# Kernel tuning notes

Measured on AMD Instinct MI355X. Metric: run time of the kernel, lower is better.

The kernel has to match this reference:

```python
import jax, jax.numpy as jnp
import numpy as np

B, T, U, V = 4, 300, 80, 1024
DE, DD, INNER = 320, 320, 512


def setup_inputs() -> dict:
    key = jax.random.key(0)
    ks = jax.random.split(key, 6)
    enc_state = jax.random.normal(ks[0], (B, T, DE), jnp.float32)
    dec_state = jax.random.normal(ks[1], (B, U + 1, DD), jnp.float32)
    Wf = jax.random.normal(ks[2], (INNER, DE + DD), jnp.float32) / np.float32(np.sqrt(DE + DD))
    bf = jnp.zeros((INNER,), jnp.float32)
    Wp = jax.random.normal(ks[3], (V, INNER), jnp.float32) / np.float32(np.sqrt(INNER))
    bp = jnp.zeros((V,), jnp.float32)
    targets = jax.random.randint(ks[4], (B, U), 1, V).astype(jnp.int32)  # labels avoid blank=0
    inputs_length = jnp.full((B,), T, jnp.int32)
    targets_length = jnp.full((B,), U, jnp.int32)
    return {"enc_state": enc_state, "dec_state": dec_state, "Wf": Wf, "bf": bf,
            "Wp": Wp, "bp": bp, "targets": targets,
            "inputs_length": inputs_length, "targets_length": targets_length}


def joint_logits(enc, dec, Wf, bf, Wp, bp):
    # Linear over concat([enc, dec]) == Linear(enc) + Linear(dec): avoids materializing the concat.
    de = enc.shape[-1]
    Wf_e, Wf_d = Wf[:, :de], Wf[:, de:]
    enc_p = jnp.einsum('btd,id->bti', enc, Wf_e)   # [B,T,inner]
    dec_p = jnp.einsum('bud,id->bui', dec, Wf_d)   # [B,U1,inner]
    h = jnp.tanh(enc_p[:, :, None, :] + dec_p[:, None, :, :] + bf)  # [B,T,U1,inner]
    return jnp.einsum('btui,vi->btuv', h, Wp) + bp  # [B,T,U1,V]


def rnnt_loss(log_probs, targets, t_len, u_len):
    # log_probs: [B,T,U1,V], blank index 0.
    lp_blank = log_probs[..., 0]  # [B,T,U1]
    lp_emit = jnp.take_along_axis(log_probs[:, :, :-1, :], targets[:, None, :, None], axis=3)[..., 0]  # [B,T,U]
    # row0: alpha[0,u] = sum_{k<u} emit[0,k]
    row0 = jnp.pad(jnp.cumsum(lp_emit[:, 0, :], axis=-1), ((0, 0), (1, 0)))  # [B,U1]

    def outer(alpha_prev, xs):
        blank_prev, emit_cur = xs  # [B,U1], [B,U]
        first = alpha_prev[:, 0] + blank_prev[:, 0]  # [B]

        def inner(c, x):
            a_plus_b, e = x  # [B],[B]
            c2 = jnp.logaddexp(a_plus_b, c + e)
            return c2, c2
        xs_in = ((alpha_prev[:, 1:] + blank_prev[:, 1:]).T, emit_cur.T)  # [U,B]
        _, rest = jax.lax.scan(inner, first, xs_in)  # [U,B]
        row = jnp.concatenate([first[None, :], rest], axis=0).T  # [B,U1]
        return row, row

    xs = (jnp.swapaxes(lp_blank[:, :-1, :], 0, 1), jnp.swapaxes(lp_emit[:, 1:, :], 0, 1))
    _, rows = jax.lax.scan(outer, row0, xs)  # [T-1,B,U1]
    alpha = jnp.concatenate([row0[None], rows], axis=0)  # [T,B,U1]
    bidx = jnp.arange(alpha.shape[1])
    ll = alpha[t_len - 1, bidx, u_len] + lp_blank[bidx, t_len - 1, u_len]
    return -jnp.mean(ll)


def reference(enc_state, dec_state, Wf, bf, Wp, bp, targets, inputs_length, targets_length):
    logits = joint_logits(enc_state, dec_state, Wf, bf, Wp, bp).astype(jnp.float32)
    log_probs = jax.nn.log_softmax(logits, axis=-1)
    return rnnt_loss(log_probs, targets, inputs_length, targets_length)
```

## Files before the change

kernel.cpp:

```cpp
#include <hip/hip_runtime.h>

#define B_DIM 4
#define T_DIM 300
#define U_DIM 80
#define UP1   81
#define V_DIM 1024
#define NINNER 512
#define NROWS (B_DIM * T_DIM * UP1)
#define EP_ROWS (B_DIM * T_DIM)
#define DP_ROWS (B_DIM * UP1)
#define NDIAG_B 380
#define NDIAG_E 379
#define WF_PART 163840
#define LOG2E 1.44269504088896341f
#define LN2   0.69314718055994531f

typedef float f32x4 __attribute__((ext_vector_type(4)));
typedef short short8 __attribute__((ext_vector_type(8)));
typedef short short4v __attribute__((ext_vector_type(4)));
typedef __bf16 bf16x8 __attribute__((ext_vector_type(8)));

static __device__ __forceinline__ short f2bf(float f) {
  return (short)__builtin_bit_cast(unsigned short, (__bf16)f);
}
static __device__ __forceinline__ float bf2f(short s) {
  unsigned int u = ((unsigned int)(unsigned short)s) << 16;
  return __builtin_bit_cast(float, u);
}
static __device__ __forceinline__ float tanh_fast(float x) {
  float e = __builtin_amdgcn_exp2f(x * 2.88539008177792681f);
  return 1.0f - 2.0f * __builtin_amdgcn_rcpf(e + 1.0f);
}
static __device__ __forceinline__ float lse2_2(float a, float b) {
  float mx = fmaxf(a, b), mn = fminf(a, b);
  return mx + __builtin_amdgcn_logf(1.0f + __builtin_amdgcn_exp2f(mn - mx));
}

__global__ __launch_bounds__(256) void cvt_kernel(
    const float* __restrict__ Wf, const float* __restrict__ Wp,
    short* __restrict__ WfB, short* __restrict__ WpB) {
  int idx = blockIdx.x * 256 + threadIdx.x;
  const int nf = (512 * 640) / 4;
  const int np = (V_DIM * NINNER) / 4;
  if (idx < nf) {
    float4 v = ((const float4*)Wf)[idx];
    int flat = idx * 4;
    int c = flat / 640;
    int kc = flat - c * 640;
    int part = (kc >= 320);
    int k0 = kc - (part ? 320 : 0);
    int dest = (part ? WF_PART : 0)
             + ((c >> 4) * 10 + (k0 >> 5)) * 512
             + (((k0 >> 3) & 3) * 16 + (c & 15)) * 8 + (k0 & 7);
    short4v o;
    o[0] = f2bf(v.x); o[1] = f2bf(v.y); o[2] = f2bf(v.z); o[3] = f2bf(v.w);
    *(short4v*)(WfB + dest) = o;
  } else if (idx < nf + np) {
    int j = idx - nf;
    float4 v = ((const float4*)Wp)[j];
    int flat = j * 4;
    int c = flat >> 9;
    int k0 = flat & 511;
    int dest = ((c >> 4) * 16 + (k0 >> 5)) * 512
             + (((k0 >> 3) & 3) * 16 + (c & 15)) * 8 + (k0 & 7);
    short4v o;
    o[0] = f2bf(v.x); o[1] = f2bf(v.y); o[2] = f2bf(v.z); o[3] = f2bf(v.w);
    *(short4v*)(WpB + dest) = o;
  }
}

#define EP_BLOCKS 19
__global__ __launch_bounds__(256) void proj_kernel(
    const float* __restrict__ enc, const float* __restrict__ dec,
    const short* __restrict__ WfB, const float* __restrict__ bfv,
    short* __restrict__ epB, short* __restrict__ dpB) {
  const int half = blockIdx.x & 1;
  const int ob = blockIdx.x >> 1;
  const bool is_dp = (ob >= EP_BLOCKS);
  const int row0 = (is_dp ? ob - EP_BLOCKS : ob) * 64;
  const int nrows = is_dp ? DP_ROWS : EP_ROWS;
  const float* __restrict__ src = is_dp ? dec : enc;
  const short* __restrict__ bb = WfB + (is_dp ? WF_PART : 0);
  short* __restrict__ out = is_dp ? dpB : epB;

  __shared__ short As[64 * 320];
  const int tid = threadIdx.x;

  #pragma unroll
  for (int it = 0; it < 10; ++it) {
    int chunk = it * 256 + tid;
    int m = chunk / 40;
    int c = chunk - m * 40;
    int r = row0 + m;
    short8 hv;
    #pragma unroll
    for (int j = 0; j < 8; ++j) hv[j] = 0;
    if (r < nrows) {
      const float* p = src + (size_t)r * 320 + c * 8;
      float4 a0 = *(const float4*)p;
      float4 a1 = *(const float4*)(p + 4);
      hv[0] = f2bf(a0.x); hv[1] = f2bf(a0.y); hv[2] = f2bf(a0.z); hv[3] = f2bf(a0.w);
      hv[4] = f2bf(a1.x); hv[5] = f2bf(a1.y); hv[6] = f2bf(a1.z); hv[7] = f2bf(a1.w);
    }
    int off = (m * 640 + c * 16) ^ ((m & 7) << 4);
    *(short8*)((char*)As + off) = hv;
  }
  __syncthreads();

  const int lane = tid & 63, wid = tid >> 6;
  const int lr = lane & 15, g = lane >> 4;

  int lin[4], xm[4];
  #pragma unroll
  for (int mf = 0; mf < 4; ++mf) {
    int row = mf * 16 + lr;
    lin[mf] = row * 640 + g * 16;
    xm[mf] = (row & 7) << 4;
  }

  const int n0 = half * 256 + wid * 64;
  const short* bptr[4];
  float bfc[4];
  #pragma unroll
  for (int nf2 = 0; nf2 < 4; ++nf2) {
    bptr[nf2] = bb + (n0 / 16 + nf2) * 5120 + lane * 8;
    bfc[nf2] = is_dp ? bfv[n0 + nf2 * 16 + lr] : 0.f;
  }
  f32x4 acc[4][4];
  #pragma unroll
  for (int mf = 0; mf < 4; ++mf)
    #pragma unroll
    for (int nf2 = 0; nf2 < 4; ++nf2)
      acc[mf][nf2] = (f32x4){0.f, 0.f, 0.f, 0.f};

  #pragma unroll 2
  for (int kk = 0; kk < 10; ++kk) {
    bf16x8 av[4], bv[4];
    #pragma unroll
    for (int mf = 0; mf < 4; ++mf) {
      int off = (lin[mf] + (kk << 6)) ^ xm[mf];
      av[mf] = __builtin_bit_cast(bf16x8, *(const short8*)((const char*)As + off));
    }
    #pragma unroll
    for (int nf2 = 0; nf2 < 4; ++nf2)
      bv[nf2] = __builtin_bit_cast(bf16x8, *(const short8*)(bptr[nf2] + kk * 512));
    #pragma unroll
    for (int mf = 0; mf < 4; ++mf)
      #pragma unroll
      for (int nf2 = 0; nf2 < 4; ++nf2)
        acc[mf][nf2] = __builtin_amdgcn_mfma_f32_16x16x32_bf16(av[mf], bv[nf2], acc[mf][nf2], 0, 0, 0);
  }
  #pragma unroll
  for (int mf = 0; mf < 4; ++mf)
    #pragma unroll
    for (int nf2 = 0; nf2 < 4; ++nf2)
      #pragma unroll
      for (int rr = 0; rr < 4; ++rr) {
        int rowl = mf * 16 + g * 4 + rr;
        int grow = row0 + rowl;
        if (grow < nrows) {
          int col = n0 + nf2 * 16 + lr;
          out[(size_t)grow * NINNER + col] = f2bf(acc[mf][nf2][rr] + bfc[nf2]);
        }
      }
}

#define JROWS 64
__global__ __launch_bounds__(512) void joint_kernel(
    const short* __restrict__ epB, const short* __restrict__ dpB,
    const short* __restrict__ WpB, const float* __restrict__ bp,
    const int* __restrict__ tgt,
    float* __restrict__ lpb_d, float* __restrict__ lpe_d) {
  extern __shared__ char hbuf[];
  __shared__ int ep_off[JROWS], dp_off[JROWS], bld_off[JROWS], eld_off[JROWS], tgt_s[JROWS];
  __shared__ float l0_s[JROWS], lt_s[JROWS];
  __shared__ float ws_s[8][JROWS];

  const int tid = threadIdx.x;
  const int row0 = blockIdx.x * JROWS;

  if (tid < JROWS) {
    int gr = row0 + tid;
    if (gr < NROWS) {
      int b = gr / (T_DIM * UP1);
      int rem = gr - b * (T_DIM * UP1);
      int t = rem / UP1;
      int u = rem - t * UP1;
      ep_off[tid] = (b * T_DIM + t) * NINNER;
      dp_off[tid] = (b * UP1 + u) * NINNER;
      bld_off[tid] = (b * NDIAG_B + (t + u)) * UP1 + u;
      eld_off[tid] = (u < U_DIM) ? ((b * NDIAG_E + (t + u)) * U_DIM + u) : -1;
      tgt_s[tid] = (u < U_DIM) ? tgt[b * U_DIM + u] : 0;
    } else {
      ep_off[tid] = 0; dp_off[tid] = 0; bld_off[tid] = -1; eld_off[tid] = -1; tgt_s[tid] = 0;
    }
    l0_s[tid] = 0.f; lt_s[tid] = 0.f;
  }
  __syncthreads();

  #pragma unroll 2
  for (int it = 0; it < 8; ++it) {
    int chunk = it * 512 + tid;
    int m = chunk >> 6, c = chunk & 63;
    short8 hv;
    #pragma unroll
    for (int j = 0; j < 8; ++j) hv[j] = 0;
    if (bld_off[m] >= 0) {
      short8 ev = *(const short8*)(epB + ep_off[m] + c * 8);
      short8 dv = *(const short8*)(dpB + dp_off[m] + c * 8);
      #pragma unroll
      for (int j = 0; j < 8; ++j)
        hv[j] = f2bf(tanh_fast(bf2f(ev[j]) + bf2f(dv[j])));
    }
    int off = ((m << 10) + (c << 4)) ^ ((m & 7) << 4);
    *(short8*)(hbuf + off) = hv;
  }
  __syncthreads();

  const int lane = tid & 63, wid = tid >> 6;
  const int lr = lane & 15, g = lane >> 4;

  int lin[4], xm[4];
  #pragma unroll
  for (int mf = 0; mf < 4; ++mf) {
    int row = mf * 16 + lr;
    lin[mf] = (row << 10) + (g << 4);
    xm[mf] = (row & 7) << 4;
  }
  int tv[4][4];
  #pragma unroll
  for (int mf = 0; mf < 4; ++mf)
    #pragma unroll
    for (int rr = 0; rr < 4; ++rr)
      tv[mf][rr] = tgt_s[mf * 16 + g * 4 + rr];

  float rsum[4][4];
  #pragma unroll
  for (int mf = 0; mf < 4; ++mf)
    #pragma unroll
    for (int rr = 0; rr < 4; ++rr) rsum[mf][rr] = 0.f;

  #pragma unroll
  for (int sc = 0; sc < 2; ++sc) {
    const int n0 = wid * 128 + sc * 64;
    const short* bptr[4];
    float bpv[4];
    #pragma unroll
    for (int nf = 0; nf < 4; ++nf) {
      bptr[nf] = WpB + (n0 / 16 + nf) * 8192 + lane * 8;
      bpv[nf] = bp[n0 + nf * 16 + lr] * LOG2E;
    }
    f32x4 acc[4][4];
    #pragma unroll
    for (int mf = 0; mf < 4; ++mf)
      #pragma unroll
      for (int nf = 0; nf < 4; ++nf)
        acc[mf][nf] = (f32x4){0.f, 0.f, 0.f, 0.f};

    #pragma unroll 2
    for (int kk = 0; kk < 16; ++kk) {
      bf16x8 av[4], bv[4];
      #pragma unroll
      for (int mf = 0; mf < 4; ++mf) {
        int off = (lin[mf] + (kk << 6)) ^ xm[mf];
        av[mf] = __builtin_bit_cast(bf16x8, *(const short8*)(hbuf + off));
      }
      #pragma unroll
      for (int nf = 0; nf < 4; ++nf)
        bv[nf] = __builtin_bit_cast(bf16x8, *(const short8*)(bptr[nf] + kk * 512));
      __builtin_amdgcn_s_setprio(1);
      #pragma unroll
      for (int mf = 0; mf < 4; ++mf)
        #pragma unroll
        for (int nf = 0; nf < 4; ++nf)
          acc[mf][nf] = __builtin_amdgcn_mfma_f32_16x16x32_bf16(av[mf], bv[nf], acc[mf][nf], 0, 0, 0);
      __builtin_amdgcn_s_setprio(0);
    }
    #pragma unroll
    for (int mf = 0; mf < 4; ++mf)
      #pragma unroll
      for (int rr = 0; rr < 4; ++rr) {
        float x0 = __builtin_fmaf(acc[mf][0][rr], LOG2E, bpv[0]);
        float x1 = __builtin_fmaf(acc[mf][1][rr], LOG2E, bpv[1]);
        float x2 = __builtin_fmaf(acc[mf][2][rr], LOG2E, bpv[2]);
        float x3 = __builtin_fmaf(acc[mf][3][rr], LOG2E, bpv[3]);
        int rowl = mf * 16 + g * 4 + rr;
        if (wid == 0 && sc == 0 && lr == 0) l0_s[rowl] = x0;
        int dtv = tv[mf][rr] - n0;
        if (dtv >= 0 && dtv < 64 && (dtv & 15) == lr) {
          int nfi = dtv >> 4;
          lt_s[rowl] = (nfi == 0) ? x0 : (nfi == 1) ? x1 : (nfi == 2) ? x2 : x3;
        }
        rsum[mf][rr] += __builtin_amdgcn_exp2f(x0) + __builtin_amdgcn_exp2f(x1)
                      + __builtin_amdgcn_exp2f(x2) + __builtin_amdgcn_exp2f(x3);
      }
  }
  #pragma unroll
  for (int mf = 0; mf < 4; ++mf)
    #pragma unroll
    for (int rr = 0; rr < 4; ++rr) {
      float s_ = rsum[mf][rr];
      #pragma unroll
      for (int o = 1; o < 16; o <<= 1) s_ += __shfl_xor(s_, o);
      if (lr == 0) ws_s[wid][mf * 16 + g * 4 + rr] = s_;
    }
  __syncthreads();
  if (tid < JROWS) {
    int bo = bld_off[tid];
    if (bo >= 0) {
      float S = 0.f;
      #pragma unroll
      for (int w = 0; w < 8; ++w) S += ws_s[w][tid];
      float lse2v = __builtin_amdgcn_logf(S);
      lpb_d[bo] = l0_s[tid] - lse2v;
      int eo = eld_off[tid];
      if (eo >= 0) lpe_d[eo] = lt_s[tid] - lse2v;
    }
  }
}

#define ACH 8
#define NCH 48
__global__ __launch_bounds__(256) void alpha_kernel(
    const float* __restrict__ lpb_d, const float* __restrict__ lpe_d,
    const int* __restrict__ ilen, const int* __restrict__ ulen_,
    float* __restrict__ out) {
  __shared__ float lls[B_DIM];
  const int tid = threadIdx.x;
  const int b = tid >> 6;
  const int lane = tid & 63;
  const float NEG = -1e30f;
  const int tl = ilen[b], ul = ulen_[b];
  const int dstar = tl - 1 + ul;

  const int u0 = lane;
  const int u1 = 64 + lane;
  const bool act1 = (u1 <= 80);
  const int uc1 = act1 ? u1 : 80;

  const float* pb = lpb_d + (size_t)b * (NDIAG_B * UP1);
  const float* pe = lpe_d + (size_t)b * (NDIAG_E * U_DIM);

  float Ab0r[ACH], Ab0m[ACH], Ae0r[ACH], Ae0m[ACH];
  float Ab1r[ACH], Ab1m[ACH], Ae1r[ACH], Ae1m[ACH];
  float Bb0r[ACH], Bb0m[ACH], Be0r[ACH], Be0m[ACH];
  float Bb1r[ACH], Bb1m[ACH], Be1r[ACH], Be1m[ACH];

  #define ALOAD(P, c)                                                        \
    {                                                                        \
      _Pragma("unroll")                                                      \
      for (int j = 0; j < ACH; ++j) {                                        \
        int dd = (c) * ACH + j;                                              \
        int ddb = dd < NDIAG_B ? dd : NDIAG_B - 1;                           \
        int dde = dd < NDIAG_E ? dd : NDIAG_E - 1;                           \
        const float* rb_ = pb + ddb * UP1;                                   \
        const float* re_ = pe + dde * U_DIM;                                 \
        P##b0r[j] = rb_[u0];                                                 \
        P##b0m[j] = rb_[u0 - 1];                                             \
        P##e0r[j] = re_[u0 - 1];                                             \
        P##e0m[j] = re_[u0 - 2];                                             \
        P##b1r[j] = rb_[uc1];                                                \
        P##b1m[j] = rb_[uc1 - 1];                                            \
        P##e1r[j] = re_[uc1 - 1];                                            \
        P##e1m[j] = re_[uc1 - 2];                                            \
      }                                                                      \
    }

  #define ACOMP(P, c)                                                        \
    {                                                                        \
      _Pragma("unroll")                                                      \
      for (int q = 0; q < ACH / 2; ++q) {                                    \
        const int j = 2 * q;                                                 \
        const int s1 = (c) * ACH + j + 1;                                    \
        float s0m1 = __shfl(pa0, (lane + 63) & 63);                          \
        float s0m2 = __shfl(pa0, (lane + 62) & 63);                          \
        float s1m1 = __shfl(pa1, (lane + 63) & 63);                          \
        float s1m2 = __shfl(pa1, (lane + 62) & 63);                          \
        float na0, na1;                                                      \
        float b1_0, e1_0, b1_1, e1_1;                                        \
        {                                                        \
          const int u = u0;                                                  \
          const int t1 = s1 - u;                                             \
          float b1 = (t1 >= 1 && t1 <= T_DIM - 1) ? P##b0r[j] : NEG;         \
          float b2 = (t1 >= 0 && t1 <= T_DIM - 2) ? P##b0r[j + 1] : NEG;     \
          float e1 = (t1 >= 0 && t1 <= T_DIM - 1 && u >= 1) ? P##e0r[j] : NEG; \
          float e2 = (t1 >= -1 && t1 <= T_DIM - 2 && u >= 1) ? P##e0r[j + 1] : NEG; \
          float b1m = (t1 >= 0 && t1 <= T_DIM - 2 && u >= 1) ? P##b0m[j] : NEG; \
          float e1m = (t1 >= -1 && t1 <= T_DIM - 2 && u >= 2) ? P##e0m[j] : NEG; \
          b1_0 = b1; e1_0 = e1;                                              \
          float T1 = b1 + b2;                                                \
          float T2 = lse2_2(e1 + b2, b1m + e2);                              \
          float T3 = e1m + e2;                                               \
          float p0 = pa0 + T1;                                               \
          float p1 = (u >= 1) ? s0m1 + T2 : NEG;                             \
          float p2 = (u >= 2) ? s0m2 + T3 : NEG;                             \
          float mx = fmaxf(fmaxf(p0, p1), p2);                               \
          float ss = __builtin_amdgcn_exp2f(p0 - mx)                         \
                   + __builtin_amdgcn_exp2f(p1 - mx)                         \
                   + __builtin_amdgcn_exp2f(p2 - mx);                        \
          na0 = mx + __builtin_amdgcn_logf(ss);                              \
        }                                                                    \
        {                                                        \
          const int t1 = s1 - u1;                                            \
          float b1 = (act1 && t1 >= 1 && t1 <= T_DIM - 1) ? P##b1r[j] : NEG; \
          float b2 = (act1 && t1 >= 0 && t1 <= T_DIM - 2) ? P##b1r[j + 1] : NEG; \
          float e1 = (act1 && t1 >= 0 && t1 <= T_DIM - 1) ? P##e1r[j] : NEG; \
          float e2 = (act1 && t1 >= -1 && t1 <= T_DIM - 2) ? P##e1r[j + 1] : NEG; \
          float b1m = (act1 && t1 >= 0 && t1 <= T_DIM - 2) ? P##b1m[j] : NEG; \
          float e1m = (act1 && t1 >= -1 && t1 <= T_DIM - 2) ? P##e1m[j] : NEG; \
          b1_1 = b1; e1_1 = e1;                                              \
          float pm1 = (lane == 0) ? s0m1 : s1m1;                             \
          float pm2 = (lane <= 1) ? s0m2 : s1m2;                             \
          float T1 = b1 + b2;                                                \
          float T2 = lse2_2(e1 + b2, b1m + e2);                              \
          float T3 = e1m + e2;                                               \
          float p0 = pa1 + T1;                                               \
          float p1 = pm1 + T2;                                               \
          float p2 = pm2 + T3;                                               \
          float mx = fmaxf(fmaxf(p0, p1), p2);                               \
          float ss = __builtin_amdgcn_exp2f(p0 - mx)                         \
                   + __builtin_amdgcn_exp2f(p1 - mx)                         \
                   + __builtin_amdgcn_exp2f(p2 - mx);                        \
          na1 = act1 ? (mx + __builtin_amdgcn_logf(ss)) : NEG;               \
        }                                                                    \
        if (s1 == dstar) {                   \
          float pm1_0 = (u0 >= 1) ? s0m1 : NEG;                              \
          float vo0 = lse2_2(pa0 + b1_0, pm1_0 + e1_0);                      \
          if (u0 == ul) fin = vo0;                                           \
          float pm1_1 = (lane == 0) ? s0m1 : s1m1;                           \
          float vo1 = lse2_2(pa1 + b1_1, pm1_1 + e1_1);                      \
          if (act1 && u1 == ul) fin = vo1;                                   \
        }                                                                    \
        pa0 = na0; pa1 = na1;                                                \
        if (s1 + 1 == dstar) {              \
          if (u0 == ul) fin = pa0;                                           \
          if (act1 && u1 == ul) fin = pa1;                                   \
        }                                                                    \
      }                                                                      \
    }

  float pa0 = (u0 == 0) ? 0.f : NEG;
  float pa1 = NEG;
  float fin = NEG;
  if (dstar == 0 && u0 == ul) fin = pa0;

  ALOAD(A, 0);
  for (int p = 0; p < NCH / 2; ++p) {
    const int cA = 2 * p, cB = 2 * p + 1;
    ALOAD(B, cB);
    ACOMP(A, cA);
    ALOAD(A, cA + 2);
    ACOMP(B, cB);
  }

  #pragma unroll
  for (int o = 32; o; o >>= 1) fin = fmaxf(fin, __shfl_xor(fin, o));
  if (lane == 0) {
    float last = pb[(size_t)dstar * UP1 + ul];
    lls[b] = fin + last;
  }
  __syncthreads();
  if (tid == 0)
    out[0] = -(lls[0] + lls[1] + lls[2] + lls[3]) * (LN2 * 0.25f);
}

extern "C" void kernel_launch(void* const* d_in, const int* in_sizes, int n_in,
                              void* d_out, int out_size, void* d_ws, size_t ws_size,
                              hipStream_t stream) {
  const float* enc = (const float*)d_in[0];
  const float* dec = (const float*)d_in[1];
  const float* Wf  = (const float*)d_in[2];
  const float* bfv = (const float*)d_in[3];
  const float* Wp  = (const float*)d_in[4];
  const float* bp  = (const float*)d_in[5];
  const int* targets = (const int*)d_in[6];
  const int* ilen    = (const int*)d_in[7];
  const int* ulen    = (const int*)d_in[8];
  float* out = (float*)d_out;
  char* ws = (char*)d_ws;

  short* WfB   = (short*)(ws + 0);
  short* WpB   = (short*)(ws + 655360);
  short* epB   = (short*)(ws + 1703936);
  short* dpB   = (short*)(ws + 2932736);
  float* lpb_d = (float*)(ws + 3264512);
  float* lpe_d = (float*)(ws + 3756992);

  cvt_kernel<<<832, 256, 0, stream>>>(Wf, Wp, WfB, WpB);
  proj_kernel<<<50, 256, 0, stream>>>(enc, dec, WfB, bfv, epB, dpB);
  joint_kernel<<<(NROWS + JROWS - 1) / JROWS, 512, 65536, stream>>>(epB, dpB, WpB, bp, targets, lpb_d, lpe_d);
  alpha_kernel<<<1, 256, 0, stream>>>(lpb_d, lpe_d, ilen, ulen, out);
}
```

Measured before the change: 225.4 us.

## Pad diagonal log-prob buffers with NEG sentinels and shrink joint tile to 48 rows

```diff
diff --git a/kernel.cpp b/kernel.cpp
--- a/kernel.cpp
+++ b/kernel.cpp
@@ -11,9 +11,11 @@
 #define DP_ROWS (B_DIM * UP1)
 #define NDIAG_B 380
 #define NDIAG_E 379
+#define DSTRIDE 82
 #define WF_PART 163840
 #define LOG2E 1.44269504088896341f
 #define LN2   0.69314718055994531f
+#define NEGF  -1e30f
 
 typedef float f32x4 __attribute__((ext_vector_type(4)));
 typedef short short8 __attribute__((ext_vector_type(8)));
@@ -34,6 +36,11 @@
 static __device__ __forceinline__ float lse2_2(float a, float b) {
   float mx = fmaxf(a, b), mn = fminf(a, b);
   return mx + __builtin_amdgcn_logf(1.0f + __builtin_amdgcn_exp2f(mn - mx));
+}
+
+__global__ __launch_bounds__(256) void fill_kernel(float* __restrict__ dst, int n4) {
+  int i = blockIdx.x * 256 + threadIdx.x;
+  if (i < n4) ((f32x4*)dst)[i] = (f32x4){NEGF, NEGF, NEGF, NEGF};
 }
 
 __global__ __launch_bounds__(256) void cvt_kernel(
@@ -165,12 +172,12 @@
       }
 }
 
-#define JROWS 64
+#define JROWS 48
 __global__ __launch_bounds__(512) void joint_kernel(
     const short* __restrict__ epB, const short* __restrict__ dpB,
     const short* __restrict__ WpB, const float* __restrict__ bp,
     const int* __restrict__ tgt,
-    float* __restrict__ lpb_d, float* __restrict__ lpe_d) {
+    float* __restrict__ lpb_p, float* __restrict__ lpe_p) {
   extern __shared__ char hbuf[];
   __shared__ int ep_off[JROWS], dp_off[JROWS], bld_off[JROWS], eld_off[JROWS], tgt_s[JROWS];
   __shared__ float l0_s[JROWS], lt_s[JROWS];
@@ -188,8 +195,8 @@
       int u = rem - t * UP1;
       ep_off[tid] = (b * T_DIM + t) * NINNER;
       dp_off[tid] = (b * UP1 + u) * NINNER;
-      bld_off[tid] = (b * NDIAG_B + (t + u)) * UP1 + u;
-      eld_off[tid] = (u < U_DIM) ? ((b * NDIAG_E + (t + u)) * U_DIM + u) : -1;
+      bld_off[tid] = (b * NDIAG_B + (t + u)) * DSTRIDE + 1 + u;
+      eld_off[tid] = (u < U_DIM) ? ((b * NDIAG_E + (t + u)) * DSTRIDE + 2 + u) : -1;
       tgt_s[tid] = (u < U_DIM) ? tgt[b * U_DIM + u] : 0;
     } else {
       ep_off[tid] = 0; dp_off[tid] = 0; bld_off[tid] = -1; eld_off[tid] = -1; tgt_s[tid] = 0;
@@ -199,7 +206,7 @@
   __syncthreads();
 
   #pragma unroll 2
-  for (int it = 0; it < 8; ++it) {
+  for (int it = 0; it < 6; ++it) {
     int chunk = it * 512 + tid;
     int m = chunk >> 6, c = chunk & 63;
     short8 hv;
@@ -220,23 +227,23 @@
   const int lane = tid & 63, wid = tid >> 6;
   const int lr = lane & 15, g = lane >> 4;
 
-  int lin[4], xm[4];
-  #pragma unroll
-  for (int mf = 0; mf < 4; ++mf) {
+  int lin[3], xm[3];
+  #pragma unroll
+  for (int mf = 0; mf < 3; ++mf) {
     int row = mf * 16 + lr;
     lin[mf] = (row << 10) + (g << 4);
     xm[mf] = (row & 7) << 4;
   }
-  int tv[4][4];
-  #pragma unroll
-  for (int mf = 0; mf < 4; ++mf)
+  int tv[3][4];
+  #pragma unroll
+  for (int mf = 0; mf < 3; ++mf)
     #pragma unroll
     for (int rr = 0; rr < 4; ++rr)
       tv[mf][rr] = tgt_s[mf * 16 + g * 4 + rr];
 
-  float rsum[4][4];
-  #pragma unroll
-  for (int mf = 0; mf < 4; ++mf)
+  float rsum[3][4];
+  #pragma unroll
+  for (int mf = 0; mf < 3; ++mf)
     #pragma unroll
     for (int rr = 0; rr < 4; ++rr) rsum[mf][rr] = 0.f;
 
@@ -250,18 +257,18 @@
       bptr[nf] = WpB + (n0 / 16 + nf) * 8192 + lane * 8;
       bpv[nf] = bp[n0 + nf * 16 + lr] * LOG2E;
     }
-    f32x4 acc[4][4];
-    #pragma unroll
-    for (int mf = 0; mf < 4; ++mf)
+    f32x4 acc[3][4];
+    #pragma unroll
+    for (int mf = 0; mf < 3; ++mf)
       #pragma unroll
       for (int nf = 0; nf < 4; ++nf)
         acc[mf][nf] = (f32x4){0.f, 0.f, 0.f, 0.f};
 
     #pragma unroll 2
     for (int kk = 0; kk < 16; ++kk) {
-      bf16x8 av[4], bv[4];
-      #pragma unroll
-      for (int mf = 0; mf < 4; ++mf) {
+      bf16x8 av[3], bv[4];
+      #pragma unroll
+      for (int mf = 0; mf < 3; ++mf) {
         int off = (lin[mf] + (kk << 6)) ^ xm[mf];
         av[mf] = __builtin_bit_cast(bf16x8, *(const short8*)(hbuf + off));
       }
@@ -270,14 +277,14 @@
         bv[nf] = __builtin_bit_cast(bf16x8, *(const short8*)(bptr[nf] + kk * 512));
       __builtin_amdgcn_s_setprio(1);
       #pragma unroll
-      for (int mf = 0; mf < 4; ++mf)
+      for (int mf = 0; mf < 3; ++mf)
         #pragma unroll
         for (int nf = 0; nf < 4; ++nf)
           acc[mf][nf] = __builtin_amdgcn_mfma_f32_16x16x32_bf16(av[mf], bv[nf], acc[mf][nf], 0, 0, 0);
       __builtin_amdgcn_s_setprio(0);
     }
     #pragma unroll
-    for (int mf = 0; mf < 4; ++mf)
+    for (int mf = 0; mf < 3; ++mf)
       #pragma unroll
       for (int rr = 0; rr < 4; ++rr) {
         float x0 = __builtin_fmaf(acc[mf][0][rr], LOG2E, bpv[0]);
@@ -296,7 +303,7 @@
       }
   }
   #pragma unroll
-  for (int mf = 0; mf < 4; ++mf)
+  for (int mf = 0; mf < 3; ++mf)
     #pragma unroll
     for (int rr = 0; rr < 4; ++rr) {
       float s_ = rsum[mf][rr];
@@ -312,9 +319,9 @@
       #pragma unroll
       for (int w = 0; w < 8; ++w) S += ws_s[w][tid];
       float lse2v = __builtin_amdgcn_logf(S);
-      lpb_d[bo] = l0_s[tid] - lse2v;
+      lpb_p[bo] = l0_s[tid] - lse2v;
       int eo = eld_off[tid];
-      if (eo >= 0) lpe_d[eo] = lt_s[tid] - lse2v;
+      if (eo >= 0) lpe_p[eo] = lt_s[tid] - lse2v;
     }
   }
 }
@@ -322,14 +329,14 @@
 #define ACH 8
 #define NCH 48
 __global__ __launch_bounds__(256) void alpha_kernel(
-    const float* __restrict__ lpb_d, const float* __restrict__ lpe_d,
+    const float* __restrict__ lpb_p, const float* __restrict__ lpe_p,
     const int* __restrict__ ilen, const int* __restrict__ ulen_,
     float* __restrict__ out) {
   __shared__ float lls[B_DIM];
   const int tid = threadIdx.x;
   const int b = tid >> 6;
   const int lane = tid & 63;
-  const float NEG = -1e30f;
+  const float NEG = NEGF;
   const int tl = ilen[b], ul = ulen_[b];
   const int dstar = tl - 1 + ul;
 
@@ -338,8 +345,8 @@
   const bool act1 = (u1 <= 80);
   const int uc1 = act1 ? u1 : 80;
 
-  const float* pb = lpb_d + (size_t)b * (NDIAG_B * UP1);
-  const float* pe = lpe_d + (size_t)b * (NDIAG_E * U_DIM);
+  const float* pbb = lpb_p + (size_t)b * (NDIAG_B * DSTRIDE);
+  const float* peb = lpe_p + (size_t)b * (NDIAG_E * DSTRIDE);
 
   float Ab0r[ACH], Ab0m[ACH], Ae0r[ACH], Ae0m[ACH];
   float Ab1r[ACH], Ab1m[ACH], Ae1r[ACH], Ae1m[ACH];
@@ -353,8 +360,8 @@
         int dd = (c) * ACH + j;                                              \
         int ddb = dd < NDIAG_B ? dd : NDIAG_B - 1;                           \
         int dde = dd < NDIAG_E ? dd : NDIAG_E - 1;                           \
-        const float* rb_ = pb + ddb * UP1;                                   \
-        const float* re_ = pe + dde * U_DIM;                                 \
+        const float* rb_ = pbb + ddb * DSTRIDE + 1;                          \
+        const float* re_ = peb + dde * DSTRIDE + 2;                          \
         P##b0r[j] = rb_[u0];                                                 \
         P##b0m[j] = rb_[u0 - 1];                                             \
         P##e0r[j] = re_[u0 - 1];                                             \
@@ -377,38 +384,26 @@
         float s1m1 = __shfl(pa1, (lane + 63) & 63);                          \
         float s1m2 = __shfl(pa1, (lane + 62) & 63);                          \
         float na0, na1;                                                      \
-        float b1_0, e1_0, b1_1, e1_1;                                        \
-        {                                                        \
-          const int u = u0;                                                  \
-          const int t1 = s1 - u;                                             \
-          float b1 = (t1 >= 1 && t1 <= T_DIM - 1) ? P##b0r[j] : NEG;         \
-          float b2 = (t1 >= 0 && t1 <= T_DIM - 2) ? P##b0r[j + 1] : NEG;     \
-          float e1 = (t1 >= 0 && t1 <= T_DIM - 1 && u >= 1) ? P##e0r[j] : NEG; \
-          float e2 = (t1 >= -1 && t1 <= T_DIM - 2 && u >= 1) ? P##e0r[j + 1] : NEG; \
-          float b1m = (t1 >= 0 && t1 <= T_DIM - 2 && u >= 1) ? P##b0m[j] : NEG; \
-          float e1m = (t1 >= -1 && t1 <= T_DIM - 2 && u >= 2) ? P##e0m[j] : NEG; \
-          b1_0 = b1; e1_0 = e1;                                              \
+        {               \
+          float b1 = P##b0r[j], b2 = P##b0r[j + 1];                          \
+          float e1 = P##e0r[j], e2 = P##e0r[j + 1];                          \
+          float b1m = P##b0m[j], e1m = P##e0m[j];                            \
           float T1 = b1 + b2;                                                \
           float T2 = lse2_2(e1 + b2, b1m + e2);                              \
           float T3 = e1m + e2;                                               \
           float p0 = pa0 + T1;                                               \
-          float p1 = (u >= 1) ? s0m1 + T2 : NEG;                             \
-          float p2 = (u >= 2) ? s0m2 + T3 : NEG;                             \
+          float p1 = s0m1 + T2;                                              \
+          float p2 = s0m2 + T3;                                              \
           float mx = fmaxf(fmaxf(p0, p1), p2);                               \
           float ss = __builtin_amdgcn_exp2f(p0 - mx)                         \
                    + __builtin_amdgcn_exp2f(p1 - mx)                         \
                    + __builtin_amdgcn_exp2f(p2 - mx);                        \
-          na0 = mx + __builtin_amdgcn_logf(ss);                              \
+          na0 = fmaxf(mx + __builtin_amdgcn_logf(ss), NEG);                  \
         }                                                                    \
         {                                                        \
-          const int t1 = s1 - u1;                                            \
-          float b1 = (act1 && t1 >= 1 && t1 <= T_DIM - 1) ? P##b1r[j] : NEG; \
-          float b2 = (act1 && t1 >= 0 && t1 <= T_DIM - 2) ? P##b1r[j + 1] : NEG; \
-          float e1 = (act1 && t1 >= 0 && t1 <= T_DIM - 1) ? P##e1r[j] : NEG; \
-          float e2 = (act1 && t1 >= -1 && t1 <= T_DIM - 2) ? P##e1r[j + 1] : NEG; \
-          float b1m = (act1 && t1 >= 0 && t1 <= T_DIM - 2) ? P##b1m[j] : NEG; \
-          float e1m = (act1 && t1 >= -1 && t1 <= T_DIM - 2) ? P##e1m[j] : NEG; \
-          b1_1 = b1; e1_1 = e1;                                              \
+          float b1 = P##b1r[j], b2 = P##b1r[j + 1];                          \
+          float e1 = P##e1r[j], e2 = P##e1r[j + 1];                          \
+          float b1m = P##b1m[j], e1m = P##e1m[j];                            \
           float pm1 = (lane == 0) ? s0m1 : s1m1;                             \
           float pm2 = (lane <= 1) ? s0m2 : s1m2;                             \
           float T1 = b1 + b2;                                                \
@@ -421,14 +416,13 @@
           float ss = __builtin_amdgcn_exp2f(p0 - mx)                         \
                    + __builtin_amdgcn_exp2f(p1 - mx)                         \
                    + __builtin_amdgcn_exp2f(p2 - mx);                        \
-          na1 = act1 ? (mx + __builtin_amdgcn_logf(ss)) : NEG;               \
+          na1 = fmaxf(mx + __builtin_amdgcn_logf(ss), NEG);                  \
         }                                                                    \
-        if (s1 == dstar) {                   \
-          float pm1_0 = (u0 >= 1) ? s0m1 : NEG;                              \
-          float vo0 = lse2_2(pa0 + b1_0, pm1_0 + e1_0);                      \
+        if (s1 == dstar) {   \
+          float vo0 = lse2_2(pa0 + P##b0r[j], s0m1 + P##e0r[j]);             \
           if (u0 == ul) fin = vo0;                                           \
-          float pm1_1 = (lane == 0) ? s0m1 : s1m1;                           \
-          float vo1 = lse2_2(pa1 + b1_1, pm1_1 + e1_1);                      \
+          float pm1c = (lane == 0) ? s0m1 : s1m1;                            \
+          float vo1 = lse2_2(pa1 + P##b1r[j], pm1c + P##e1r[j]);             \
           if (act1 && u1 == ul) fin = vo1;                                   \
         }                                                                    \
         pa0 = na0; pa1 = na1;                                                \
@@ -456,7 +450,7 @@
   #pragma unroll
   for (int o = 32; o; o >>= 1) fin = fmaxf(fin, __shfl_xor(fin, o));
   if (lane == 0) {
-    float last = pb[(size_t)dstar * UP1 + ul];
+    float last = pbb[(size_t)dstar * DSTRIDE + 1 + ul];
     lls[b] = fin + last;
   }
   __syncthreads();
@@ -483,11 +477,13 @@
   short* WpB   = (short*)(ws + 655360);
   short* epB   = (short*)(ws + 1703936);
   short* dpB   = (short*)(ws + 2932736);
-  float* lpb_d = (float*)(ws + 3264512);
-  float* lpe_d = (float*)(ws + 3756992);
-
+  float* lpb_p = (float*)(ws + 3264512);
+  float* lpe_p = (float*)(ws + 3763072);
+  const int FILL_N4 = (4 * NDIAG_B * DSTRIDE + 4 * NDIAG_E * DSTRIDE) / 4;
+
+  fill_kernel<<<(FILL_N4 + 255) / 256, 256, 0, stream>>>(lpb_p, FILL_N4);
   cvt_kernel<<<832, 256, 0, stream>>>(Wf, Wp, WfB, WpB);
   proj_kernel<<<50, 256, 0, stream>>>(enc, dec, WfB, bfv, epB, dpB);
-  joint_kernel<<<(NROWS + JROWS - 1) / JROWS, 512, 65536, stream>>>(epB, dpB, WpB, bp, targets, lpb_d, lpe_d);
-  alpha_kernel<<<1, 256, 0, stream>>>(lpb_d, lpe_d, ilen, ulen, out);
-}
+  joint_kernel<<<NROWS / JROWS, 512, 49152, stream>>>(epB, dpB, WpB, bp, targets, lpb_p, lpe_p);
+  alpha_kernel<<<1, 256, 0, stream>>>(lpb_p, lpe_p, ilen, ulen, out);
+}
```

Result: slower. 234.5 us (+4.1%).
